# Performance work log

Measured on AMD Instinct MI355X. Metric: run time of the kernel, lower is better.

The kernel has to match this reference:

```python
import jax, jax.numpy as jnp
import numpy as np

N_SPATIAL = 3          # config.N_spatial_dim
N_POL = 2              # config.N_polarizations
DT = 0.1               # config.simulation_config.dt
EPS = 1e-8

N_NODES = 100000
N_EDGES = 1600000
IN_DIM = 16
MSG_DIM = 128


def setup_inputs() -> dict:
    key = jax.random.key(0)
    ks = jax.random.split(key, 6)
    x = jax.random.normal(ks[0], (N_NODES, IN_DIM), dtype=jnp.float32)
    edge_index = jax.random.randint(ks[1], (2, N_EDGES), 0, N_NODES, dtype=jnp.int64)
    W_msg = jax.random.normal(ks[2], (IN_DIM, MSG_DIM), dtype=jnp.float32) * (1.0 / np.sqrt(IN_DIM))
    b_msg = jax.random.normal(ks[3], (MSG_DIM,), dtype=jnp.float32) * 0.01
    W_out = jax.random.normal(ks[4], (MSG_DIM, IN_DIM), dtype=jnp.float32) * (1.0 / np.sqrt(MSG_DIM))
    b_out = jax.random.normal(ks[5], (IN_DIM,), dtype=jnp.float32) * 0.01
    return {"x": x, "edge_index": edge_index, "W_msg": W_msg, "b_msg": b_msg,
            "W_out": W_out, "b_out": b_out, "steps": 4}


def _step(x, src, dst, W_msg, b_msg, W_out, b_out):
    # message_conv: per-node transform, gather at source, scatter-sum at destination
    h = x @ W_msg + b_msg                                   # [N, MSG_DIM]
    messages = jax.ops.segment_sum(h[src], dst, num_segments=N_NODES)  # [N, MSG_DIM]
    # message_to_output: Linear(MSG_DIM -> IN_DIM)
    output = messages @ W_out + b_out                       # [N, IN_DIM]
    # update: residual Euler step + L2-normalize polarization slice
    x = x + output * DT
    start, end = N_SPATIAL, N_SPATIAL + 2 * N_POL
    pol = x[:, start:end]
    norm = jnp.sqrt(jnp.sum(pol * pol, axis=1, keepdims=True))
    pol = pol / jnp.maximum(norm, EPS)                      # F.normalize(p=2, eps=1e-8)
    return jnp.concatenate((x[:, :start], pol, x[:, end:]), axis=1)


def reference(x, edge_index, W_msg, b_msg, W_out, b_out, steps):
    src, dst = edge_index[0], edge_index[1]
    for _ in range(steps):
        x = _step(x, src, dst, W_msg, b_msg, W_out, b_out)
    return x
```

## Files before the change

kernel.cpp:

```cpp
#include <hip/hip_runtime.h>

#define NN 100000
#define NE 1600000
#define IN_DIM 16
#define MSG_DIM 128
#define DT_C 0.1f
#define EPS_C 1e-8f
#define BKT 128
#define NB ((NN + BKT - 1) / BKT)
#define EPB 2560
#define NBB (NE / EPB)
#define EPT (EPB / 256)
#define CAPB 4096
#define CAP 2560

__device__ __forceinline__ float blo(unsigned c) { return __uint_as_float(c << 16); }
__device__ __forceinline__ float bhi(unsigned c) { return __uint_as_float(c & 0xFFFF0000u); }
__device__ __forceinline__ unsigned short f2b(float f) {
    unsigned int i = __float_as_uint(f);
    unsigned int b = i + 0x7FFFu + ((i >> 16) & 1u);
    return (unsigned short)(b >> 16);
}

__global__ void init_kernel(const float* __restrict__ W_msg,
                            const float* __restrict__ b_msg,
                            const float* __restrict__ W_out,
                            const float* __restrict__ x,
                            float* __restrict__ Wc,
                            float* __restrict__ bc,
                            unsigned* __restrict__ xb,
                            int* __restrict__ gcur) {
    int t = threadIdx.x;
    if (blockIdx.x == 0) {
        int i = t >> 4, j = t & 15;
        float s = 0.f;
        for (int k = 0; k < MSG_DIM; ++k)
            s += W_msg[i * MSG_DIM + k] * W_out[k * IN_DIM + j];
        Wc[t] = s;
        if (t < IN_DIM) {
            float sb = 0.f;
            for (int k = 0; k < MSG_DIM; ++k)
                sb += b_msg[k] * W_out[k * IN_DIM + t];
            bc[t] = sb;
        }
    }
    int i = blockIdx.x * blockDim.x + t;
    if (i < NB) gcur[i] = i * CAPB;
    if (i * 2 < NN * IN_DIM) {
        float2 v = ((const float2*)x)[i];
        xb[i] = (unsigned)f2b(v.x) | ((unsigned)f2b(v.y) << 16);
    }
}

__global__ __launch_bounds__(256) void bucketA_kernel(const int* __restrict__ src,
                                                      const int* __restrict__ dst,
                                                      int* __restrict__ gcur,
                                                      unsigned* __restrict__ bucket) {
    __shared__ int lcnt[NB];
    __shared__ int lbase[NB];
    int t = threadIdx.x;
    for (int j = t; j < NB; j += 256) lcnt[j] = 0;
    __syncthreads();

    int d[EPT], s[EPT];
    int base = blockIdx.x * EPB + t;
    #pragma unroll
    for (int it = 0; it < EPT; ++it) {
        d[it] = dst[base + it * 256];
        s[it] = src[base + it * 256];
    }
    #pragma unroll
    for (int it = 0; it < EPT; ++it) atomicAdd(&lcnt[d[it] >> 7], 1);
    __syncthreads();
    for (int j = t; j < NB; j += 256) {
        int c = lcnt[j];
        lbase[j] = c ? atomicAdd(&gcur[j], c) : 0;
        lcnt[j] = 0;
    }
    __syncthreads();
    #pragma unroll
    for (int it = 0; it < EPT; ++it) {
        int b = d[it] >> 7;
        int slot = atomicAdd(&lcnt[b], 1);
        bucket[lbase[b] + slot] = ((unsigned)(d[it] & 127) << 17) | (unsigned)s[it];
    }
}

__global__ __launch_bounds__(256) void bucket2csr_kernel(const unsigned* __restrict__ bucket,
                                                         const int* __restrict__ gcur,
                                                         unsigned* __restrict__ offs,
                                                         int* __restrict__ csr) {
    __shared__ int lcnt[BKT];
    __shared__ int ls[BKT];
    __shared__ int lcur[BKT];
    __shared__ int lcsr[CAP];
    int b = blockIdx.x;
    int t = threadIdx.x;
    int p0 = b * CAPB;
    int len = gcur[b] - p0;
    if (t < BKT) lcnt[t] = 0;
    __syncthreads();
    for (int i = t; i < len; i += 256)
        atomicAdd(&lcnt[bucket[p0 + i] >> 17], 1);
    __syncthreads();
    if (t < BKT) ls[t] = lcnt[t];
    __syncthreads();
    #pragma unroll
    for (int off = 1; off < BKT; off <<= 1) {
        int u = (t < BKT && t >= off) ? ls[t - off] : 0;
        __syncthreads();
        if (t < BKT) ls[t] += u;
        __syncthreads();
    }
    if (t < BKT) {
        int ex = ls[t] - lcnt[t];
        lcur[t] = ex;
        int n = b * BKT + t;
        if (n < NN) {
            unsigned dgc = (unsigned)(lcnt[t] > 1023 ? 1023 : lcnt[t]);
            offs[n] = ((unsigned)(p0 + ex) << 10) | dgc;
        }
    }
    __syncthreads();
    if (len <= CAP) {
        for (int i = t; i < len; i += 256) {
            unsigned pk = bucket[p0 + i];
            int pos = atomicAdd(&lcur[pk >> 17], 1);
            lcsr[pos] = (int)(pk & 0x1FFFFu);
        }
        __syncthreads();
        for (int i = t; i < len; i += 256) csr[p0 + i] = lcsr[i];
    } else {
        for (int i = t; i < len; i += 256) {
            unsigned pk = bucket[p0 + i];
            int pos = atomicAdd(&lcur[pk >> 17], 1);
            csr[p0 + pos] = (int)(pk & 0x1FFFFu);
        }
    }
}

__global__ __launch_bounds__(256) void step_kernel(const float2* __restrict__ x2in,
                                                   const uint4* __restrict__ xbin,
                                                   const unsigned* __restrict__ offs,
                                                   const int* __restrict__ csr,
                                                   const float* __restrict__ Wc,
                                                   const float* __restrict__ bc,
                                                   const float* __restrict__ b_out,
                                                   float2* __restrict__ x2out,
                                                   unsigned* __restrict__ xbout) {
    __shared__ float sWc[256];
    __shared__ float sbc[16];
    __shared__ float sb[16];
    int t = threadIdx.x;
    sWc[t] = Wc[t];
    if (t < 16) { sbc[t] = bc[t]; sb[t] = b_out[t]; }
    __syncthreads();

    int tid = blockIdx.x * 256 + t;
    int n = tid >> 3;
    int l = t & 7;
    int p = l >> 1;
    int hf = l & 1;
    if (n >= NN) return;

    unsigned po = offs[n];
    int o0 = (int)(po >> 10);
    int deg = (int)(po & 1023u);
    int o1 = o0 + deg;

    float acc[8];
    #pragma unroll
    for (int j = 0; j < 8; ++j) acc[j] = 0.f;

    int e = o0 + p;
    while (e + 4 < o1) {
        int s0 = csr[e];
        int s1 = csr[e + 4];
        uint4 v0 = xbin[s0 * 2 + hf];
        uint4 v1 = xbin[s1 * 2 + hf];
        acc[0] += blo(v0.x); acc[1] += bhi(v0.x);
        acc[2] += blo(v0.y); acc[3] += bhi(v0.y);
        acc[4] += blo(v0.z); acc[5] += bhi(v0.z);
        acc[6] += blo(v0.w); acc[7] += bhi(v0.w);
        acc[0] += blo(v1.x); acc[1] += bhi(v1.x);
        acc[2] += blo(v1.y); acc[3] += bhi(v1.y);
        acc[4] += blo(v1.z); acc[5] += bhi(v1.z);
        acc[6] += blo(v1.w); acc[7] += bhi(v1.w);
        e += 8;
    }
    if (e < o1) {
        int s0 = csr[e];
        uint4 v0 = xbin[s0 * 2 + hf];
        acc[0] += blo(v0.x); acc[1] += bhi(v0.x);
        acc[2] += blo(v0.y); acc[3] += bhi(v0.y);
        acc[4] += blo(v0.z); acc[5] += bhi(v0.z);
        acc[6] += blo(v0.w); acc[7] += bhi(v0.w);
    }

    #pragma unroll
    for (int j = 0; j < 8; ++j) {
        acc[j] += __shfl_xor(acc[j], 2);
        acc[j] += __shfl_xor(acc[j], 4);
    }
    float a[16];
    #pragma unroll
    for (int j = 0; j < 8; ++j) {
        float oth = __shfl_xor(acc[j], 1);
        a[j]     = hf ? oth    : acc[j];
        a[8 + j] = hf ? acc[j] : oth;
    }

    float dg = (float)deg;

    int c0 = 2 * l;
    float o0f = dg * sbc[c0] + sb[c0];
    float o1f = dg * sbc[c0 + 1] + sb[c0 + 1];
    #pragma unroll
    for (int k = 0; k < 16; ++k) {
        float ak = a[k];
        o0f = fmaf(ak, sWc[k * 16 + c0], o0f);
        o1f = fmaf(ak, sWc[k * 16 + c0 + 1], o1f);
    }

    float2 xv = x2in[(size_t)n * 8 + l];
    float xn0 = xv.x + DT_C * o0f;
    float xn1 = xv.y + DT_C * o1f;

    bool in0 = (c0 >= 3 && c0 <= 6);
    bool in1 = (c0 + 1 >= 3 && c0 + 1 <= 6);
    float ssp = (in0 ? xn0 * xn0 : 0.f) + (in1 ? xn1 * xn1 : 0.f);
    ssp += __shfl_xor(ssp, 1);
    ssp += __shfl_xor(ssp, 2);
    ssp += __shfl_xor(ssp, 4);
    float sc = 1.0f / fmaxf(sqrtf(ssp), EPS_C);
    if (in0) xn0 *= sc;
    if (in1) xn1 *= sc;

    x2out[(size_t)n * 8 + l] = make_float2(xn0, xn1);
    xbout[(size_t)n * 8 + l] = (unsigned)f2b(xn0) | ((unsigned)f2b(xn1) << 16);
}

extern "C" void kernel_launch(void* const* d_in, const int* in_sizes, int n_in,
                              void* d_out, int out_size, void* d_ws, size_t ws_size,
                              hipStream_t stream) {
    const float* x0    = (const float*)d_in[0];
    const int*   ei    = (const int*)d_in[1];
    const float* W_msg = (const float*)d_in[2];
    const float* b_msg = (const float*)d_in[3];
    const float* W_out = (const float*)d_in[4];
    const float* b_out = (const float*)d_in[5];

    float* X = (float*)d_out;

    float*          Y      = (float*)d_ws;
    unsigned*       xb0    = (unsigned*)(Y + (size_t)NN * IN_DIM);
    unsigned*       xb1    = xb0 + (size_t)NN * (IN_DIM / 2);
    unsigned*       bucket = xb1 + (size_t)NN * (IN_DIM / 2);
    int*            csr    = (int*)(bucket + (size_t)NB * CAPB);
    unsigned*       offs   = (unsigned*)(csr + (size_t)NB * CAPB);
    int*            gcur   = (int*)(offs + NN);
    float*          Wc     = (float*)(gcur + NB);
    float*          bc     = Wc + 256;

    const int* src = ei;
    const int* dst = ei + NE;

    init_kernel<<<(NN * IN_DIM / 2 + 255) / 256, 256, 0, stream>>>(
        W_msg, b_msg, W_out, x0, Wc, bc, xb0, gcur);
    bucketA_kernel<<<NBB, 256, 0, stream>>>(src, dst, gcur, bucket);
    bucket2csr_kernel<<<NB, 256, 0, stream>>>(bucket, gcur, offs, csr);

    const int step_threads = NN * 8;
    const int step_blocks = (step_threads + 255) / 256;

    const float*    fin[4]  = { x0,  Y,   X,   Y  };
    float*          fout[4] = { Y,   X,   Y,   X  };
    const unsigned* bin[4]  = { xb0, xb1, xb0, xb1 };
    unsigned*       bout[4] = { xb1, xb0, xb1, xb0 };
    for (int s = 0; s < 4; ++s) {
        step_kernel<<<step_blocks, 256, 0, stream>>>(
            (const float2*)fin[s], (const uint4*)bin[s], offs, csr,
            Wc, bc, b_out, (float2*)fout[s], bout[s]);
    }
}
```

Baseline: 122.6 us.

## Pad CSR rows to even length and drop fp32 state between steps

Each destination's CSR segment is padded to an even length with a dummy node (index NN) whose bf16 row is zeroed, so the gather loop can read source pairs as int2 with no tail handling. The residual input now comes from the bf16 buffer instead of a separate fp32 copy, and fp32 output is written only on the last step. This cuts gather and state traffic per step, but the residual carries bf16 rounding across steps, which may hurt accuracy. The padding also takes a little extra CSR space, and segments can overflow the local shared-memory path.

```diff
diff --git a/kernel.cpp b/kernel.cpp
--- a/kernel.cpp
+++ b/kernel.cpp
@@ -28,7 +28,8 @@
                             const float* __restrict__ x,
                             float* __restrict__ Wc,
                             float* __restrict__ bc,
-                            unsigned* __restrict__ xb,
+                            unsigned* __restrict__ xb0,
+                            unsigned* __restrict__ xb1,
                             int* __restrict__ gcur) {
     int t = threadIdx.x;
     if (blockIdx.x == 0) {
@@ -46,9 +47,12 @@
     }
     int i = blockIdx.x * blockDim.x + t;
     if (i < NB) gcur[i] = i * CAPB;
-    if (i * 2 < NN * IN_DIM) {
+    if (i < NN * (IN_DIM / 2)) {
         float2 v = ((const float2*)x)[i];
-        xb[i] = (unsigned)f2b(v.x) | ((unsigned)f2b(v.y) << 16);
+        xb0[i] = (unsigned)f2b(v.x) | ((unsigned)f2b(v.y) << 16);
+    } else if (i < (NN + 1) * (IN_DIM / 2)) {
+        xb0[i] = 0u;
+        xb1[i] = 0u;
     }
 }
 
@@ -103,7 +107,8 @@
     for (int i = t; i < len; i += 256)
         atomicAdd(&lcnt[bucket[p0 + i] >> 17], 1);
     __syncthreads();
-    if (t < BKT) ls[t] = lcnt[t];
+    int pd = 0;
+    if (t < BKT) { pd = lcnt[t] + (lcnt[t] & 1); ls[t] = pd; }
     __syncthreads();
     #pragma unroll
     for (int off = 1; off < BKT; off <<= 1) {
@@ -113,41 +118,46 @@
         __syncthreads();
     }
     if (t < BKT) {
-        int ex = ls[t] - lcnt[t];
-        lcur[t] = ex;
+        int pex = ls[t] - pd;
+        lcur[t] = pex;
         int n = b * BKT + t;
         if (n < NN) {
             unsigned dgc = (unsigned)(lcnt[t] > 1023 ? 1023 : lcnt[t]);
-            offs[n] = ((unsigned)(p0 + ex) << 10) | dgc;
-        }
-    }
-    __syncthreads();
-    if (len <= CAP) {
+            offs[n] = ((unsigned)(p0 + pex) << 10) | dgc;
+        }
+    }
+    __syncthreads();
+    int padtot = ls[BKT - 1];
+    if (padtot <= CAP) {
         for (int i = t; i < len; i += 256) {
             unsigned pk = bucket[p0 + i];
             int pos = atomicAdd(&lcur[pk >> 17], 1);
             lcsr[pos] = (int)(pk & 0x1FFFFu);
         }
         __syncthreads();
-        for (int i = t; i < len; i += 256) csr[p0 + i] = lcsr[i];
+        if (t < BKT && (lcnt[t] & 1)) lcsr[lcur[t]] = NN;
+        __syncthreads();
+        for (int i = t; i < padtot; i += 256) csr[p0 + i] = lcsr[i];
     } else {
         for (int i = t; i < len; i += 256) {
             unsigned pk = bucket[p0 + i];
             int pos = atomicAdd(&lcur[pk >> 17], 1);
             csr[p0 + pos] = (int)(pk & 0x1FFFFu);
         }
-    }
-}
-
-__global__ __launch_bounds__(256) void step_kernel(const float2* __restrict__ x2in,
-                                                   const uint4* __restrict__ xbin,
+        __syncthreads();
+        if (t < BKT && (lcnt[t] & 1)) csr[p0 + lcur[t]] = NN;
+    }
+}
+
+__global__ __launch_bounds__(256) void step_kernel(const uint4* __restrict__ xbin,
                                                    const unsigned* __restrict__ offs,
-                                                   const int* __restrict__ csr,
+                                                   const int2* __restrict__ csr2,
                                                    const float* __restrict__ Wc,
                                                    const float* __restrict__ bc,
                                                    const float* __restrict__ b_out,
+                                                   unsigned* __restrict__ xbout,
                                                    float2* __restrict__ x2out,
-                                                   unsigned* __restrict__ xbout) {
+                                                   int last) {
     __shared__ float sWc[256];
     __shared__ float sbc[16];
     __shared__ float sb[16];
@@ -166,18 +176,18 @@
     unsigned po = offs[n];
     int o0 = (int)(po >> 10);
     int deg = (int)(po & 1023u);
-    int o1 = o0 + deg;
+    int pdeg = deg + (deg & 1);
+    int e2beg = (o0 >> 1) + p;
+    int e2end = (o0 + pdeg) >> 1;
 
     float acc[8];
     #pragma unroll
     for (int j = 0; j < 8; ++j) acc[j] = 0.f;
 
-    int e = o0 + p;
-    while (e + 4 < o1) {
-        int s0 = csr[e];
-        int s1 = csr[e + 4];
-        uint4 v0 = xbin[s0 * 2 + hf];
-        uint4 v1 = xbin[s1 * 2 + hf];
+    for (int e2 = e2beg; e2 < e2end; e2 += 4) {
+        int2 ss = csr2[e2];
+        uint4 v0 = xbin[ss.x * 2 + hf];
+        uint4 v1 = xbin[ss.y * 2 + hf];
         acc[0] += blo(v0.x); acc[1] += bhi(v0.x);
         acc[2] += blo(v0.y); acc[3] += bhi(v0.y);
         acc[4] += blo(v0.z); acc[5] += bhi(v0.z);
@@ -186,15 +196,6 @@
         acc[2] += blo(v1.y); acc[3] += bhi(v1.y);
         acc[4] += blo(v1.z); acc[5] += bhi(v1.z);
         acc[6] += blo(v1.w); acc[7] += bhi(v1.w);
-        e += 8;
-    }
-    if (e < o1) {
-        int s0 = csr[e];
-        uint4 v0 = xbin[s0 * 2 + hf];
-        acc[0] += blo(v0.x); acc[1] += bhi(v0.x);
-        acc[2] += blo(v0.y); acc[3] += bhi(v0.y);
-        acc[4] += blo(v0.z); acc[5] += bhi(v0.z);
-        acc[6] += blo(v0.w); acc[7] += bhi(v0.w);
     }
 
     #pragma unroll
@@ -222,9 +223,9 @@
         o1f = fmaf(ak, sWc[k * 16 + c0 + 1], o1f);
     }
 
-    float2 xv = x2in[(size_t)n * 8 + l];
-    float xn0 = xv.x + DT_C * o0f;
-    float xn1 = xv.y + DT_C * o1f;
+    unsigned ox = ((const unsigned*)xbin)[(size_t)n * 8 + l];
+    float xn0 = blo(ox) + DT_C * o0f;
+    float xn1 = bhi(ox) + DT_C * o1f;
 
     bool in0 = (c0 >= 3 && c0 <= 6);
     bool in1 = (c0 + 1 >= 3 && c0 + 1 <= 6);
@@ -236,8 +237,11 @@
     if (in0) xn0 *= sc;
     if (in1) xn1 *= sc;
 
-    x2out[(size_t)n * 8 + l] = make_float2(xn0, xn1);
-    xbout[(size_t)n * 8 + l] = (unsigned)f2b(xn0) | ((unsigned)f2b(xn1) << 16);
+    if (last) {
+        x2out[(size_t)n * 8 + l] = make_float2(xn0, xn1);
+    } else {
+        xbout[(size_t)n * 8 + l] = (unsigned)f2b(xn0) | ((unsigned)f2b(xn1) << 16);
+    }
 }
 
 extern "C" void kernel_launch(void* const* d_in, const int* in_sizes, int n_in,
@@ -252,34 +256,31 @@
 
     float* X = (float*)d_out;
 
-    float*          Y      = (float*)d_ws;
-    unsigned*       xb0    = (unsigned*)(Y + (size_t)NN * IN_DIM);
-    unsigned*       xb1    = xb0 + (size_t)NN * (IN_DIM / 2);
-    unsigned*       bucket = xb1 + (size_t)NN * (IN_DIM / 2);
-    int*            csr    = (int*)(bucket + (size_t)NB * CAPB);
-    unsigned*       offs   = (unsigned*)(csr + (size_t)NB * CAPB);
-    int*            gcur   = (int*)(offs + NN);
-    float*          Wc     = (float*)(gcur + NB);
-    float*          bc     = Wc + 256;
+    unsigned* xb0    = (unsigned*)d_ws;
+    unsigned* xb1    = xb0 + (size_t)(NN + 1) * (IN_DIM / 2);
+    unsigned* bucket = xb1 + (size_t)(NN + 1) * (IN_DIM / 2);
+    int*      csr    = (int*)(bucket + (size_t)NB * CAPB);
+    unsigned* offs   = (unsigned*)(csr + (size_t)NB * CAPB);
+    int*      gcur   = (int*)(offs + NN);
+    float*    Wc     = (float*)(gcur + NB);
+    float*    bc     = Wc + 256;
 
     const int* src = ei;
     const int* dst = ei + NE;
 
-    init_kernel<<<(NN * IN_DIM / 2 + 255) / 256, 256, 0, stream>>>(
-        W_msg, b_msg, W_out, x0, Wc, bc, xb0, gcur);
+    init_kernel<<<((NN + 1) * (IN_DIM / 2) + 255) / 256, 256, 0, stream>>>(
+        W_msg, b_msg, W_out, x0, Wc, bc, xb0, xb1, gcur);
     bucketA_kernel<<<NBB, 256, 0, stream>>>(src, dst, gcur, bucket);
     bucket2csr_kernel<<<NB, 256, 0, stream>>>(bucket, gcur, offs, csr);
 
     const int step_threads = NN * 8;
     const int step_blocks = (step_threads + 255) / 256;
 
-    const float*    fin[4]  = { x0,  Y,   X,   Y  };
-    float*          fout[4] = { Y,   X,   Y,   X  };
     const unsigned* bin[4]  = { xb0, xb1, xb0, xb1 };
     unsigned*       bout[4] = { xb1, xb0, xb1, xb0 };
     for (int s = 0; s < 4; ++s) {
         step_kernel<<<step_blocks, 256, 0, stream>>>(
-            (const float2*)fin[s], (const uint4*)bin[s], offs, csr,
-            Wc, bc, b_out, (float2*)fout[s], bout[s]);
-    }
-}
+            (const uint4*)bin[s], offs, (const int2*)csr,
+            Wc, bc, b_out, bout[s], (float2*)X, (s == 3) ? 1 : 0);
+    }
+}
```

New measurement: 117.4 us, median of 2. 1.04x faster.
